# Optimization experiments

Hardware: AMD Instinct MI355X
Metric: run time of the kernel (lower is better)

The kernel has to match this reference:

```python
import jax, jax.numpy as jnp
import numpy as np

B, L, H = 32, 512, 1024
Q = 128
VA_H = 256

def setup_inputs() -> dict:
    key = jax.random.key(0)
    ks = jax.random.split(key, 12)
    hidden_states = jax.random.normal(ks[0], (B, L, H), dtype=jnp.float32)
    # Build valid inclusive spans: start in [2, L-16), length in [0, 8)
    asp_s = jax.random.randint(ks[1], (B, Q), 2, L - 16)
    asp_e = asp_s + jax.random.randint(ks[2], (B, Q), 0, 8)
    opi_s = jax.random.randint(ks[3], (B, Q), 2, L - 16)
    opi_e = opi_s + jax.random.randint(ks[4], (B, Q), 0, 8)
    null = jax.random.uniform(ks[5], (B, Q)) < 0.1
    asp_s = jnp.where(null, 0, asp_s)
    quad_spans = jnp.stack([asp_s, asp_e, opi_s, opi_e], axis=-1).astype(jnp.int64)
    quad_mask = (jax.random.uniform(ks[6], (B, Q)) > 0.3).astype(jnp.float32)
    # MLP params (torch Linear: y = x @ W.T + b), kaiming-ish scale
    def lin(k, out_d, in_d):
        return jax.random.normal(k, (out_d, in_d), dtype=jnp.float32) / np.sqrt(in_d)
    W1 = lin(ks[7], VA_H, 3 * H); b1 = jnp.zeros((VA_H,), jnp.float32)
    W2 = lin(ks[8], VA_H // 2, VA_H); b2 = jnp.zeros((VA_H // 2,), jnp.float32)
    W3 = lin(ks[9], 2, VA_H // 2); b3 = jnp.zeros((2,), jnp.float32)
    return {"hidden_states": hidden_states, "quad_spans": quad_spans,
            "quad_mask": quad_mask, "W1": W1, "b1": b1, "W2": W2, "b2": b2,
            "W3": W3, "b3": b3}

def _pool_spans(hidden_states, s, e):
    # hidden_states: [B,L,H]; s,e: [B,Q] inclusive indices
    pos = jnp.arange(hidden_states.shape[1])  # [L]
    valid = (s >= 2) & (e >= s)               # [B,Q]
    m = (pos[None, None, :] >= s[..., None]) & (pos[None, None, :] <= e[..., None])
    m = (m & valid[..., None]).astype(hidden_states.dtype)  # [B,Q,L]
    cnt = jnp.maximum(m.sum(-1, keepdims=True), 1.0)        # [B,Q,1]
    mean = jnp.einsum('bql,blh->bqh', m, hidden_states) / cnt
    sep = hidden_states[:, 1:2, :]                           # [B,1,H] fallback
    return jnp.where(valid[..., None], mean, sep)

def reference(hidden_states, quad_spans, quad_mask, W1, b1, W2, b2, W3, b3):
    h_asp = _pool_spans(hidden_states, quad_spans[..., 0], quad_spans[..., 1])
    h_opi = _pool_spans(hidden_states, quad_spans[..., 2], quad_spans[..., 3])
    h_pair = jnp.concatenate([h_asp, h_opi, h_asp * h_opi], axis=-1)  # [B,Q,3H]
    x = jax.nn.gelu(h_pair @ W1.T + b1, approximate=False)  # torch GELU = erf
    x = jax.nn.gelu(x @ W2.T + b2, approximate=False)
    va = jax.nn.sigmoid(x @ W3.T + b3) * 8.0 + 1.0          # [B,Q,2] in [1,9]
    # Invalid pairs stay zero, matching the torch loop's skipped entries
    return va * (quad_mask >= 0.5).astype(va.dtype)[..., None]
```

## Files before the change

### kernel.cpp

```cpp
#include <hip/hip_runtime.h>
#include <hip/hip_bf16.h>
#include <math.h>

#define Bn 32
#define Ln 512
#define Hn 1024
#define Qn 128

typedef __bf16 bf16x8 __attribute__((ext_vector_type(8)));
typedef float f32x4 __attribute__((ext_vector_type(4)));

__device__ __forceinline__ unsigned short f2bf(float x) {
    union { float f; unsigned int u; } v; v.f = x;
    unsigned int r = v.u + 0x7fffu + ((v.u >> 16) & 1u);
    return (unsigned short)(r >> 16);
}
__device__ __forceinline__ float gelu_exact(float v) {
    return 0.5f * v * (1.0f + erff(v * 0.70710678118654752f));
}

__global__ __launch_bounds__(256) void pool_kernel(const float* __restrict__ hs,
                                                   const int* __restrict__ spans,
                                                   unsigned short* __restrict__ hp) {
    const int pair = blockIdx.x;
    const int b = pair >> 7;
    const int tid = threadIdx.x;

    const bool is64 = (spans[1] == 0);
    int s_a, e_a, s_o, e_o;
    if (is64) {
        s_a = spans[(pair * 4 + 0) * 2]; e_a = spans[(pair * 4 + 1) * 2];
        s_o = spans[(pair * 4 + 2) * 2]; e_o = spans[(pair * 4 + 3) * 2];
    } else {
        s_a = spans[pair * 4 + 0]; e_a = spans[pair * 4 + 1];
        s_o = spans[pair * 4 + 2]; e_o = spans[pair * 4 + 3];
    }

    const float4* base = (const float4*)hs + (size_t)b * Ln * (Hn / 4);

    float4 A, O;
    if (s_a >= 2 && e_a >= s_a) {
        float sx = 0.f, sy = 0.f, sz = 0.f, sw = 0.f;
        for (int t = s_a; t <= e_a; ++t) {
            float4 v = base[t * (Hn / 4) + tid];
            sx += v.x; sy += v.y; sz += v.z; sw += v.w;
        }
        float inv = 1.0f / (float)(e_a - s_a + 1);
        A.x = sx * inv; A.y = sy * inv; A.z = sz * inv; A.w = sw * inv;
    } else {
        A = base[(Hn / 4) + tid];
    }
    if (s_o >= 2 && e_o >= s_o) {
        float sx = 0.f, sy = 0.f, sz = 0.f, sw = 0.f;
        for (int t = s_o; t <= e_o; ++t) {
            float4 v = base[t * (Hn / 4) + tid];
            sx += v.x; sy += v.y; sz += v.z; sw += v.w;
        }
        float inv = 1.0f / (float)(e_o - s_o + 1);
        O.x = sx * inv; O.y = sy * inv; O.z = sz * inv; O.w = sw * inv;
    } else {
        O = base[(Hn / 4) + tid];
    }

    unsigned short* row = hp + (size_t)pair * 3072;
    const int d = tid * 4;
    ushort4 pa, po, pp;
    pa.x = f2bf(A.x); pa.y = f2bf(A.y); pa.z = f2bf(A.z); pa.w = f2bf(A.w);
    po.x = f2bf(O.x); po.y = f2bf(O.y); po.z = f2bf(O.z); po.w = f2bf(O.w);
    pp.x = f2bf(A.x * O.x); pp.y = f2bf(A.y * O.y);
    pp.z = f2bf(A.z * O.z); pp.w = f2bf(A.w * O.w);
    *(ushort4*)(row + d) = pa;
    *(ushort4*)(row + 1024 + d) = po;
    *(ushort4*)(row + 2048 + d) = pp;
}

__global__ __launch_bounds__(256, 4) void gemm1_pipe(const unsigned short* __restrict__ A,
                                                     const float* __restrict__ Wf,
                                                     float* __restrict__ xacc,
                                                     int M, int N, int K, int Ks) {
    __shared__ __align__(16) unsigned short As[2][64][72];
    __shared__ __align__(16) unsigned short Bs[2][64][72];

    const int tid = threadIdx.x;
    const int lane = tid & 63;
    const int wid = tid >> 6;
    const int wM = (wid >> 1) * 32;
    const int wN = (wid & 1) * 32;
    const int quad = lane >> 4;
    const int l16 = lane & 15;
    const int m0 = blockIdx.x * 64;
    const int n0 = blockIdx.y * 64;
    const int kb0 = blockIdx.z * Ks;
    const int r = tid >> 3;
    const int c = (tid & 7) * 8;

    const unsigned short* Ap0 = A + (size_t)(m0 + r) * K + kb0 + c;
    const unsigned short* Ap1 = Ap0 + (size_t)32 * K;
    const float* Bp0 = Wf + (size_t)(n0 + r) * K + kb0 + c;
    const float* Bp1 = Bp0 + (size_t)32 * K;

    uint4 ra0, ra1;
    float4 rb0, rb1, rb2, rb3;

    ra0 = *(const uint4*)Ap0;
    ra1 = *(const uint4*)Ap1;
    rb0 = *(const float4*)Bp0; rb1 = *(const float4*)(Bp0 + 4);
    rb2 = *(const float4*)Bp1; rb3 = *(const float4*)(Bp1 + 4);
    {
        *(uint4*)&As[0][r][c] = ra0;
        *(uint4*)&As[0][r + 32][c] = ra1;
        ushort4 u;
        u.x = f2bf(rb0.x); u.y = f2bf(rb0.y); u.z = f2bf(rb0.z); u.w = f2bf(rb0.w);
        *(ushort4*)&Bs[0][r][c] = u;
        u.x = f2bf(rb1.x); u.y = f2bf(rb1.y); u.z = f2bf(rb1.z); u.w = f2bf(rb1.w);
        *(ushort4*)&Bs[0][r][c + 4] = u;
        u.x = f2bf(rb2.x); u.y = f2bf(rb2.y); u.z = f2bf(rb2.z); u.w = f2bf(rb2.w);
        *(ushort4*)&Bs[0][r + 32][c] = u;
        u.x = f2bf(rb3.x); u.y = f2bf(rb3.y); u.z = f2bf(rb3.z); u.w = f2bf(rb3.w);
        *(ushort4*)&Bs[0][r + 32][c + 4] = u;
    }

    f32x4 acc[2][2] = {};
    const int iters = Ks / 64;

    for (int it = 0; it < iters; ++it) {
        const int buf = it & 1;
        __syncthreads();
        if (it + 1 < iters) {
            const int off = (it + 1) * 64;
            ra0 = *(const uint4*)(Ap0 + off);
            ra1 = *(const uint4*)(Ap1 + off);
            rb0 = *(const float4*)(Bp0 + off); rb1 = *(const float4*)(Bp0 + off + 4);
            rb2 = *(const float4*)(Bp1 + off); rb3 = *(const float4*)(Bp1 + off + 4);
        }
#pragma unroll
        for (int kk = 0; kk < 64; kk += 32) {
            bf16x8 a0 = *(const bf16x8*)&As[buf][wM + l16][kk + quad * 8];
            bf16x8 a1 = *(const bf16x8*)&As[buf][wM + 16 + l16][kk + quad * 8];
            bf16x8 b0 = *(const bf16x8*)&Bs[buf][wN + l16][kk + quad * 8];
            bf16x8 b1 = *(const bf16x8*)&Bs[buf][wN + 16 + l16][kk + quad * 8];
            acc[0][0] = __builtin_amdgcn_mfma_f32_16x16x32_bf16(a0, b0, acc[0][0], 0, 0, 0);
            acc[0][1] = __builtin_amdgcn_mfma_f32_16x16x32_bf16(a0, b1, acc[0][1], 0, 0, 0);
            acc[1][0] = __builtin_amdgcn_mfma_f32_16x16x32_bf16(a1, b0, acc[1][0], 0, 0, 0);
            acc[1][1] = __builtin_amdgcn_mfma_f32_16x16x32_bf16(a1, b1, acc[1][1], 0, 0, 0);
        }
        if (it + 1 < iters) {
            const int nb = buf ^ 1;
            *(uint4*)&As[nb][r][c] = ra0;
            *(uint4*)&As[nb][r + 32][c] = ra1;
            ushort4 u;
            u.x = f2bf(rb0.x); u.y = f2bf(rb0.y); u.z = f2bf(rb0.z); u.w = f2bf(rb0.w);
            *(ushort4*)&Bs[nb][r][c] = u;
            u.x = f2bf(rb1.x); u.y = f2bf(rb1.y); u.z = f2bf(rb1.z); u.w = f2bf(rb1.w);
            *(ushort4*)&Bs[nb][r][c + 4] = u;
            u.x = f2bf(rb2.x); u.y = f2bf(rb2.y); u.z = f2bf(rb2.z); u.w = f2bf(rb2.w);
            *(ushort4*)&Bs[nb][r + 32][c] = u;
            u.x = f2bf(rb3.x); u.y = f2bf(rb3.y); u.z = f2bf(rb3.z); u.w = f2bf(rb3.w);
            *(ushort4*)&Bs[nb][r + 32][c + 4] = u;
        }
    }

#pragma unroll
    for (int mi = 0; mi < 2; ++mi) {
#pragma unroll
        for (int ni = 0; ni < 2; ++ni) {
            const int n = n0 + wN + ni * 16 + l16;
#pragma unroll
            for (int rr = 0; rr < 4; ++rr) {
                const int m = m0 + wM + mi * 16 + quad * 4 + rr;
                unsafeAtomicAdd(&xacc[(size_t)m * N + n], acc[mi][ni][rr]);
            }
        }
    }
}

__global__ __launch_bounds__(256) void gelu_bias(const float* __restrict__ xacc,
                                                 const float* __restrict__ bias,
                                                 unsigned short* __restrict__ xout,
                                                 int total4, int ncols4) {
    for (int i = blockIdx.x * blockDim.x + threadIdx.x; i < total4;
         i += gridDim.x * blockDim.x) {
        float4 v = ((const float4*)xacc)[i];
        float4 bv = ((const float4*)bias)[i & (ncols4 - 1)];
        ushort4 u;
        u.x = f2bf(gelu_exact(v.x + bv.x));
        u.y = f2bf(gelu_exact(v.y + bv.y));
        u.z = f2bf(gelu_exact(v.z + bv.z));
        u.w = f2bf(gelu_exact(v.w + bv.w));
        ((ushort4*)xout)[i] = u;
    }
}

__global__ __launch_bounds__(256) void mlp2_head(const unsigned short* __restrict__ x1,
                                                 const float* __restrict__ W2f,
                                                 const float* __restrict__ b2,
                                                 const float* __restrict__ W3,
                                                 const float* __restrict__ b3,
                                                 const float* __restrict__ mask,
                                                 float* __restrict__ out) {
    __shared__ __align__(16) unsigned short Xs[32][72];
    __shared__ __align__(16) unsigned short Ws[128][72];
    __shared__ float X2[32][132];

    const int tid = threadIdx.x;
    const int lane = tid & 63;
    const int wid = tid >> 6;
    const int wM = (wid >> 1) * 16;
    const int wN = (wid & 1) * 64;
    const int quad = lane >> 4;
    const int l16 = lane & 15;
    const int m0 = blockIdx.x * 32;

    f32x4 acc[4] = {};

    for (int k0 = 0; k0 < 256; k0 += 64) {
        {
            const int r = tid >> 3, c = (tid & 7) * 8;
            *(uint4*)&Xs[r][c] = *(const uint4*)(x1 + (size_t)(m0 + r) * 256 + k0 + c);
        }
#pragma unroll
        for (int p = 0; p < 4; ++p) {
            const int v = tid + p * 256;
            const int r = v >> 3, c = (v & 7) * 8;
            const float* src = W2f + (size_t)r * 256 + k0 + c;
            float4 f0 = *(const float4*)src;
            float4 f1 = *(const float4*)(src + 4);
            ushort4 u;
            u.x = f2bf(f0.x); u.y = f2bf(f0.y); u.z = f2bf(f0.z); u.w = f2bf(f0.w);
            *(ushort4*)&Ws[r][c] = u;
            u.x = f2bf(f1.x); u.y = f2bf(f1.y); u.z = f2bf(f1.z); u.w = f2bf(f1.w);
            *(ushort4*)&Ws[r][c + 4] = u;
        }
        __syncthreads();
#pragma unroll
        for (int kk = 0; kk < 64; kk += 32) {
            bf16x8 a = *(const bf16x8*)&Xs[wM + l16][kk + quad * 8];
#pragma unroll
            for (int ni = 0; ni < 4; ++ni) {
                bf16x8 b = *(const bf16x8*)&Ws[wN + ni * 16 + l16][kk + quad * 8];
                acc[ni] = __builtin_amdgcn_mfma_f32_16x16x32_bf16(a, b, acc[ni], 0, 0, 0);
            }
        }
        __syncthreads();
    }

#pragma unroll
    for (int ni = 0; ni < 4; ++ni) {
        const int n = wN + ni * 16 + l16;
        const float bn = b2[n];
#pragma unroll
        for (int rr = 0; rr < 4; ++rr) {
            const int m = wM + quad * 4 + rr;
            X2[m][n] = gelu_exact(acc[ni][rr] + bn);
        }
    }
    __syncthreads();

    const int p = tid >> 3;
    const int cc = (tid & 7) * 16;
    float a0 = 0.f, a1 = 0.f;
#pragma unroll
    for (int j = 0; j < 16; ++j) {
        const float xv = X2[p][cc + j];
        a0 += xv * W3[cc + j];
        a1 += xv * W3[128 + cc + j];
    }
    a0 += __shfl_xor(a0, 1); a0 += __shfl_xor(a0, 2); a0 += __shfl_xor(a0, 4);
    a1 += __shfl_xor(a1, 1); a1 += __shfl_xor(a1, 2); a1 += __shfl_xor(a1, 4);
    if ((tid & 7) == 0) {
        const int pair = m0 + p;
        const float mk = (mask[pair] >= 0.5f) ? 1.0f : 0.0f;
        out[pair * 2 + 0] = ((1.0f / (1.0f + expf(-(a0 + b3[0])))) * 8.0f + 1.0f) * mk;
        out[pair * 2 + 1] = ((1.0f / (1.0f + expf(-(a1 + b3[1])))) * 8.0f + 1.0f) * mk;
    }
}

extern "C" void kernel_launch(void* const* d_in, const int* in_sizes, int n_in,
                              void* d_out, int out_size, void* d_ws, size_t ws_size,
                              hipStream_t stream) {
    const float* hs   = (const float*)d_in[0];
    const int*   spans= (const int*)d_in[1];
    const float* mask = (const float*)d_in[2];
    const float* W1   = (const float*)d_in[3];
    const float* b1   = (const float*)d_in[4];
    const float* W2   = (const float*)d_in[5];
    const float* b2   = (const float*)d_in[6];
    const float* W3   = (const float*)d_in[7];
    const float* b3   = (const float*)d_in[8];
    float* out = (float*)d_out;

    unsigned short* hp    = (unsigned short*)d_ws;
    float*          xacc1 = (float*)((char*)d_ws + 25165824);
    unsigned short* x1    = (unsigned short*)d_ws;

    hipMemsetAsync(xacc1, 0, (size_t)4096 * 256 * 4, stream);
    pool_kernel<<<dim3(4096), dim3(256), 0, stream>>>(hs, spans, hp);
    gemm1_pipe<<<dim3(64, 4, 4), dim3(256), 0, stream>>>(hp, W1, xacc1, 4096, 256, 3072, 768);
    gelu_bias<<<dim3(512), dim3(256), 0, stream>>>(xacc1, b1, x1, 4096 * 256 / 4, 64);
    mlp2_head<<<dim3(128), dim3(256), 0, stream>>>(x1, W2, b2, W3, b3, mask, out);
}
```

Measured before the change: 160.3 us.

## Pre-convert W1 to bf16 and use 128x128 GEMM tiles with direct LDS loads

A combined prep kernel now pools the spans, converts W1 to bf16 once, and zeroes the accumulator, which replaces the separate memset. GEMM1 moves to 128x128 tiles with a 4x4 MFMA block per wave, an XOR-swizzled LDS layout, and global_load_lds direct-to-LDS loads, with split-K raised to 8. This removes the per-tile fp32-to-bf16 conversion of W1 and raises data reuse per tile. The cost is a loss of software double buffering: each of the 6 K-steps now loads, syncs and computes serially. The higher split-K also doubles the atomic traffic into the accumulator.

```diff
diff --git a/kernel.cpp b/kernel.cpp
--- a/kernel.cpp
+++ b/kernel.cpp
@@ -1,11 +1,6 @@
 #include <hip/hip_runtime.h>
 #include <hip/hip_bf16.h>
 #include <math.h>
-
-#define Bn 32
-#define Ln 512
-#define Hn 1024
-#define Qn 128
 
 typedef __bf16 bf16x8 __attribute__((ext_vector_type(8)));
 typedef float f32x4 __attribute__((ext_vector_type(4)));
@@ -19,12 +14,31 @@
     return 0.5f * v * (1.0f + erff(v * 0.70710678118654752f));
 }
 
-__global__ __launch_bounds__(256) void pool_kernel(const float* __restrict__ hs,
+__global__ __launch_bounds__(256) void prep_kernel(const float* __restrict__ hs,
                                                    const int* __restrict__ spans,
-                                                   unsigned short* __restrict__ hp) {
-    const int pair = blockIdx.x;
+                                                   const float* __restrict__ W1,
+                                                   unsigned short* __restrict__ hp,
+                                                   unsigned short* __restrict__ w1b,
+                                                   float* __restrict__ xacc1) {
+    const int blk = blockIdx.x;
+    const int tid = threadIdx.x;
+
+    if (blk >= 4096) {
+        if (blk < 4864) {
+            const int i = (blk - 4096) * 256 + tid;
+            float4 f = ((const float4*)W1)[i];
+            ushort4 u;
+            u.x = f2bf(f.x); u.y = f2bf(f.y); u.z = f2bf(f.z); u.w = f2bf(f.w);
+            ((ushort4*)w1b)[i] = u;
+        } else {
+            const int i = (blk - 4864) * 256 + tid;
+            ((float4*)xacc1)[i] = make_float4(0.f, 0.f, 0.f, 0.f);
+        }
+        return;
+    }
+
+    const int pair = blk;
     const int b = pair >> 7;
-    const int tid = threadIdx.x;
 
     const bool is64 = (spans[1] == 0);
     int s_a, e_a, s_o, e_o;
@@ -36,30 +50,30 @@
         s_o = spans[pair * 4 + 2]; e_o = spans[pair * 4 + 3];
     }
 
-    const float4* base = (const float4*)hs + (size_t)b * Ln * (Hn / 4);
+    const float4* base = (const float4*)hs + (size_t)b * 512 * 256;
 
     float4 A, O;
     if (s_a >= 2 && e_a >= s_a) {
         float sx = 0.f, sy = 0.f, sz = 0.f, sw = 0.f;
         for (int t = s_a; t <= e_a; ++t) {
-            float4 v = base[t * (Hn / 4) + tid];
+            float4 v = base[t * 256 + tid];
             sx += v.x; sy += v.y; sz += v.z; sw += v.w;
         }
         float inv = 1.0f / (float)(e_a - s_a + 1);
         A.x = sx * inv; A.y = sy * inv; A.z = sz * inv; A.w = sw * inv;
     } else {
-        A = base[(Hn / 4) + tid];
+        A = base[256 + tid];
     }
     if (s_o >= 2 && e_o >= s_o) {
         float sx = 0.f, sy = 0.f, sz = 0.f, sw = 0.f;
         for (int t = s_o; t <= e_o; ++t) {
-            float4 v = base[t * (Hn / 4) + tid];
+            float4 v = base[t * 256 + tid];
             sx += v.x; sy += v.y; sz += v.z; sw += v.w;
         }
         float inv = 1.0f / (float)(e_o - s_o + 1);
         O.x = sx * inv; O.y = sy * inv; O.z = sz * inv; O.w = sw * inv;
     } else {
-        O = base[(Hn / 4) + tid];
+        O = base[256 + tid];
     }
 
     unsigned short* row = hp + (size_t)pair * 3072;
@@ -74,101 +88,85 @@
     *(ushort4*)(row + 2048 + d) = pp;
 }
 
-__global__ __launch_bounds__(256, 4) void gemm1_pipe(const unsigned short* __restrict__ A,
-                                                     const float* __restrict__ Wf,
-                                                     float* __restrict__ xacc,
-                                                     int M, int N, int K, int Ks) {
-    __shared__ __align__(16) unsigned short As[2][64][72];
-    __shared__ __align__(16) unsigned short Bs[2][64][72];
+__global__ __launch_bounds__(256, 2) void gemm1_mfma(const unsigned short* __restrict__ A,
+                                                     const unsigned short* __restrict__ Bw,
+                                                     float* __restrict__ xacc) {
+    __shared__ __align__(16) unsigned short As[128 * 64];
+    __shared__ __align__(16) unsigned short Bs[128 * 64];
 
     const int tid = threadIdx.x;
     const int lane = tid & 63;
     const int wid = tid >> 6;
-    const int wM = (wid >> 1) * 32;
-    const int wN = (wid & 1) * 32;
     const int quad = lane >> 4;
     const int l16 = lane & 15;
-    const int m0 = blockIdx.x * 64;
-    const int n0 = blockIdx.y * 64;
-    const int kb0 = blockIdx.z * Ks;
-    const int r = tid >> 3;
-    const int c = (tid & 7) * 8;
-
-    const unsigned short* Ap0 = A + (size_t)(m0 + r) * K + kb0 + c;
-    const unsigned short* Ap1 = Ap0 + (size_t)32 * K;
-    const float* Bp0 = Wf + (size_t)(n0 + r) * K + kb0 + c;
-    const float* Bp1 = Bp0 + (size_t)32 * K;
-
-    uint4 ra0, ra1;
-    float4 rb0, rb1, rb2, rb3;
-
-    ra0 = *(const uint4*)Ap0;
-    ra1 = *(const uint4*)Ap1;
-    rb0 = *(const float4*)Bp0; rb1 = *(const float4*)(Bp0 + 4);
-    rb2 = *(const float4*)Bp1; rb3 = *(const float4*)(Bp1 + 4);
-    {
-        *(uint4*)&As[0][r][c] = ra0;
-        *(uint4*)&As[0][r + 32][c] = ra1;
-        ushort4 u;
-        u.x = f2bf(rb0.x); u.y = f2bf(rb0.y); u.z = f2bf(rb0.z); u.w = f2bf(rb0.w);
-        *(ushort4*)&Bs[0][r][c] = u;
-        u.x = f2bf(rb1.x); u.y = f2bf(rb1.y); u.z = f2bf(rb1.z); u.w = f2bf(rb1.w);
-        *(ushort4*)&Bs[0][r][c + 4] = u;
-        u.x = f2bf(rb2.x); u.y = f2bf(rb2.y); u.z = f2bf(rb2.z); u.w = f2bf(rb2.w);
-        *(ushort4*)&Bs[0][r + 32][c] = u;
-        u.x = f2bf(rb3.x); u.y = f2bf(rb3.y); u.z = f2bf(rb3.z); u.w = f2bf(rb3.w);
-        *(ushort4*)&Bs[0][r + 32][c + 4] = u;
-    }
-
-    f32x4 acc[2][2] = {};
-    const int iters = Ks / 64;
-
-    for (int it = 0; it < iters; ++it) {
-        const int buf = it & 1;
-        __syncthreads();
-        if (it + 1 < iters) {
-            const int off = (it + 1) * 64;
-            ra0 = *(const uint4*)(Ap0 + off);
-            ra1 = *(const uint4*)(Ap1 + off);
-            rb0 = *(const float4*)(Bp0 + off); rb1 = *(const float4*)(Bp0 + off + 4);
-            rb2 = *(const float4*)(Bp1 + off); rb3 = *(const float4*)(Bp1 + off + 4);
-        }
-#pragma unroll
-        for (int kk = 0; kk < 64; kk += 32) {
-            bf16x8 a0 = *(const bf16x8*)&As[buf][wM + l16][kk + quad * 8];
-            bf16x8 a1 = *(const bf16x8*)&As[buf][wM + 16 + l16][kk + quad * 8];
-            bf16x8 b0 = *(const bf16x8*)&Bs[buf][wN + l16][kk + quad * 8];
-            bf16x8 b1 = *(const bf16x8*)&Bs[buf][wN + 16 + l16][kk + quad * 8];
-            acc[0][0] = __builtin_amdgcn_mfma_f32_16x16x32_bf16(a0, b0, acc[0][0], 0, 0, 0);
-            acc[0][1] = __builtin_amdgcn_mfma_f32_16x16x32_bf16(a0, b1, acc[0][1], 0, 0, 0);
-            acc[1][0] = __builtin_amdgcn_mfma_f32_16x16x32_bf16(a1, b0, acc[1][0], 0, 0, 0);
-            acc[1][1] = __builtin_amdgcn_mfma_f32_16x16x32_bf16(a1, b1, acc[1][1], 0, 0, 0);
-        }
-        if (it + 1 < iters) {
-            const int nb = buf ^ 1;
-            *(uint4*)&As[nb][r][c] = ra0;
-            *(uint4*)&As[nb][r + 32][c] = ra1;
-            ushort4 u;
-            u.x = f2bf(rb0.x); u.y = f2bf(rb0.y); u.z = f2bf(rb0.z); u.w = f2bf(rb0.w);
-            *(ushort4*)&Bs[nb][r][c] = u;
-            u.x = f2bf(rb1.x); u.y = f2bf(rb1.y); u.z = f2bf(rb1.z); u.w = f2bf(rb1.w);
-            *(ushort4*)&Bs[nb][r][c + 4] = u;
-            u.x = f2bf(rb2.x); u.y = f2bf(rb2.y); u.z = f2bf(rb2.z); u.w = f2bf(rb2.w);
-            *(ushort4*)&Bs[nb][r + 32][c] = u;
-            u.x = f2bf(rb3.x); u.y = f2bf(rb3.y); u.z = f2bf(rb3.z); u.w = f2bf(rb3.w);
-            *(ushort4*)&Bs[nb][r + 32][c + 4] = u;
-        }
-    }
-
-#pragma unroll
-    for (int mi = 0; mi < 2; ++mi) {
-#pragma unroll
-        for (int ni = 0; ni < 2; ++ni) {
+    const int wM = (wid >> 1) * 64;
+    const int wN = (wid & 1) * 64;
+    const int m0 = blockIdx.x * 128;
+    const int n0 = blockIdx.y * 128;
+    const int kb = blockIdx.z * 384;
+
+    const int srow = tid >> 3;
+    const int lchunk = (tid & 7) ^ (srow & 7);
+    const unsigned short* Abase = A + (size_t)(m0 + srow) * 3072 + kb + lchunk * 8;
+    const unsigned short* Bbase = Bw + (size_t)(n0 + srow) * 3072 + kb + lchunk * 8;
+
+    int aoff[4][2], boff[4][2];
+#pragma unroll
+    for (int mi = 0; mi < 4; ++mi) {
+#pragma unroll
+        for (int h = 0; h < 2; ++h) {
+            int row = wM + mi * 16 + l16;
+            int pc = (h * 4 + quad) ^ (row & 7);
+            aoff[mi][h] = row * 64 + pc * 8;
+            row = wN + mi * 16 + l16;
+            pc = (h * 4 + quad) ^ (row & 7);
+            boff[mi][h] = row * 64 + pc * 8;
+        }
+    }
+
+    f32x4 acc[4][4] = {};
+
+#pragma unroll
+    for (int it = 0; it < 6; ++it) {
+        const int kadv = it * 64;
+#pragma unroll
+        for (int j = 0; j < 4; ++j) {
+            __builtin_amdgcn_global_load_lds(
+                (const __attribute__((address_space(1))) void*)(Abase + (size_t)j * 32 * 3072 + kadv),
+                (__attribute__((address_space(3))) void*)(&As[(j * 256 + tid) * 8]),
+                16, 0, 0);
+            __builtin_amdgcn_global_load_lds(
+                (const __attribute__((address_space(1))) void*)(Bbase + (size_t)j * 32 * 3072 + kadv),
+                (__attribute__((address_space(3))) void*)(&Bs[(j * 256 + tid) * 8]),
+                16, 0, 0);
+        }
+        __syncthreads();
+#pragma unroll
+        for (int h = 0; h < 2; ++h) {
+            bf16x8 af[4], bfr[4];
+#pragma unroll
+            for (int mi = 0; mi < 4; ++mi) af[mi] = *(const bf16x8*)&As[aoff[mi][h]];
+#pragma unroll
+            for (int ni = 0; ni < 4; ++ni) bfr[ni] = *(const bf16x8*)&Bs[boff[ni][h]];
+#pragma unroll
+            for (int mi = 0; mi < 4; ++mi)
+#pragma unroll
+                for (int ni = 0; ni < 4; ++ni)
+                    acc[mi][ni] = __builtin_amdgcn_mfma_f32_16x16x32_bf16(
+                        af[mi], bfr[ni], acc[mi][ni], 0, 0, 0);
+        }
+        __syncthreads();
+    }
+
+#pragma unroll
+    for (int mi = 0; mi < 4; ++mi) {
+#pragma unroll
+        for (int ni = 0; ni < 4; ++ni) {
             const int n = n0 + wN + ni * 16 + l16;
 #pragma unroll
             for (int rr = 0; rr < 4; ++rr) {
                 const int m = m0 + wM + mi * 16 + quad * 4 + rr;
-                unsafeAtomicAdd(&xacc[(size_t)m * N + n], acc[mi][ni][rr]);
+                unsafeAtomicAdd(&xacc[(size_t)m * 256 + n], acc[mi][ni][rr]);
             }
         }
     }
@@ -291,11 +289,11 @@
 
     unsigned short* hp    = (unsigned short*)d_ws;
     float*          xacc1 = (float*)((char*)d_ws + 25165824);
+    unsigned short* w1b   = (unsigned short*)((char*)d_ws + 29360128);
     unsigned short* x1    = (unsigned short*)d_ws;
 
-    hipMemsetAsync(xacc1, 0, (size_t)4096 * 256 * 4, stream);
-    pool_kernel<<<dim3(4096), dim3(256), 0, stream>>>(hs, spans, hp);
-    gemm1_pipe<<<dim3(64, 4, 4), dim3(256), 0, stream>>>(hp, W1, xacc1, 4096, 256, 3072, 768);
+    prep_kernel<<<dim3(5888), dim3(256), 0, stream>>>(hs, spans, W1, hp, w1b, xacc1);
+    gemm1_mfma<<<dim3(32, 2, 8), dim3(256), 0, stream>>>(hp, w1b, xacc1);
     gelu_bias<<<dim3(512), dim3(256), 0, stream>>>(xacc1, b1, x1, 4096 * 256 / 4, 64);
     mlp2_head<<<dim3(128), dim3(256), 0, stream>>>(x1, W2, b2, W3, b3, mask, out);
 }
```

Measured after the change: 166.4 us. 1.04x slower.
